# Kernel tuning notes

Measured on AMD Instinct MI355X. Metric: run time of the kernel, lower is better.

## Reference

```python
import jax, jax.numpy as jnp
import numpy as np

EMBED_DIM = 1024
NUM_HEAD = 16
HEAD_DIM = EMBED_DIM // NUM_HEAD


def _linear_params(key, in_dim, out_dim):
    kw, kb = jax.random.split(key)
    bound = 1.0 / np.sqrt(in_dim)
    W = jax.random.uniform(kw, (out_dim, in_dim), minval=-bound, maxval=bound, dtype=jnp.float32)
    b = jax.random.uniform(kb, (out_dim,), minval=-bound, maxval=bound, dtype=jnp.float32)
    return W, b


def setup_inputs() -> dict:
    key = jax.random.key(0)
    ks = jax.random.split(key, 7)
    N, S, E = 2, 2048, EMBED_DIM
    k = jax.random.normal(ks[0], (N, S, E), dtype=jnp.float32)
    q = jax.random.normal(ks[1], (N, S, E), dtype=jnp.float32)
    v = jax.random.normal(ks[2], (N, S, E), dtype=jnp.float32)
    Wk, bk = _linear_params(ks[3], E, E)
    Wq, bq = _linear_params(ks[4], E, E)
    Wv, bv = _linear_params(ks[5], E, E)
    Wo, bo = _linear_params(ks[6], E, E)
    return {"key": k, "query": q, "value": v,
            "Wk": Wk, "bk": bk, "Wq": Wq, "bq": bq,
            "Wv": Wv, "bv": bv, "Wo": Wo, "bo": bo}


def reference(key, query, value, Wk, bk, Wq, bq, Wv, bv, Wo, bo):
    N, S_in, E = key.shape
    S_out = query.shape[1]
    H, D = NUM_HEAD, HEAD_DIM
    # projections (torch Linear: x @ W.T + b), split heads -> [N, H, S, D]
    k = (key @ Wk.T + bk).reshape(N, S_in, H, D).transpose(0, 2, 1, 3)
    q = (query @ Wq.T + bq).reshape(N, S_out, H, D).transpose(0, 2, 1, 3)
    v = (value @ Wv.T + bv).reshape(N, S_in, H, D).transpose(0, 2, 1, 3)
    # unfused attention: full [N,H,S_out,S_in] score matrix, scale, softmax
    weight = jnp.einsum("nhqd,nhkd->nhqk", q, k) / jnp.sqrt(jnp.float32(D))
    weight = jax.nn.softmax(weight, axis=-1)
    attn = jnp.einsum("nhqk,nhkd->nhqd", weight, v)  # [N,H,S_out,D]
    attn = attn.transpose(0, 2, 1, 3).reshape(N, S_out, E)
    return attn @ Wo.T + bo
```

## Files before the change

### kernel.cpp

```cpp
#include <hip/hip_runtime.h>

constexpr int E  = 1024;
constexpr int NH = 16;
constexpr int HD = 64;
constexpr int S  = 2048;
constexpr int NB = 2;
constexpr int M  = NB * S;

typedef unsigned short u16;
typedef _Float16 f16;
typedef __attribute__((ext_vector_type(8))) _Float16 h8v;
typedef __attribute__((ext_vector_type(2))) __fp16 hp2v;
typedef __attribute__((ext_vector_type(4))) float f4v;

__device__ __forceinline__ f4v mfmaH(h8v a, h8v b, f4v c) {
    return __builtin_amdgcn_mfma_f32_16x16x32_f16(a, b, c, 0, 0, 0);
}
__device__ __forceinline__ u16 f16bits(float x) {
    union { f16 h; u16 u; } t; t.h = (f16)x; return t.u;
}
__device__ __forceinline__ unsigned pkrtz(float a, float b) {
    union { hp2v h; unsigned u; } t;
    t.h = __builtin_amdgcn_cvt_pkrtz(a, b);
    return t.u;
}
__device__ __forceinline__ float fexp2(float x) {
    float r;
    asm("v_exp_f32 %0, %1" : "=v"(r) : "v"(x));
    return r;
}
typedef const __attribute__((address_space(1))) void gvoid;
typedef __attribute__((address_space(3))) void lvoid;
__device__ __forceinline__ void load_lds16(const u16* g, u16* l) {
    __builtin_amdgcn_global_load_lds((gvoid*)g, (lvoid*)l, 16, 0, 0);
}

__global__ __launch_bounds__(256)
void cvt_f16(const float* __restrict__ q, const float* __restrict__ k,
             const float* __restrict__ v,
             const float* __restrict__ wq, const float* __restrict__ wk,
             const float* __restrict__ wv, const float* __restrict__ wo,
             u16* __restrict__ out)
{
    const size_t ME = (size_t)M * E, EE = (size_t)E * E;
    const int z = blockIdx.y;
    const float* src = (z == 0) ? q : (z == 1) ? k : (z == 2) ? v
                     : (z == 3) ? wq : (z == 4) ? wk : (z == 5) ? wv : wo;
    const size_t len = (z < 3) ? ME : EE;
    u16* dst = out + ((z < 3) ? (size_t)z * ME : 3 * ME + (size_t)(z - 3) * EE);
    for (size_t i = ((size_t)blockIdx.x * 256 + threadIdx.x) * 8; i < len;
         i += (size_t)gridDim.x * 256 * 8) {
        float4 a = *reinterpret_cast<const float4*>(src + i);
        float4 b = *reinterpret_cast<const float4*>(src + i + 4);
        h8v o;
        o[0] = (f16)a.x; o[1] = (f16)a.y; o[2] = (f16)a.z; o[3] = (f16)a.w;
        o[4] = (f16)b.x; o[5] = (f16)b.y; o[6] = (f16)b.z; o[7] = (f16)b.w;
        *reinterpret_cast<h8v*>(dst + i) = o;
    }
}

__device__ __forceinline__ void gemm16_core(const u16* __restrict__ A,
                                            const u16* __restrict__ W,
                                            int bm, int bn, u16* lds, f4v acc[4][4])
{
    const int tid  = threadIdx.x;
    const int lane = tid & 63;
    const int wid  = tid >> 6;
    const int g = lane >> 4, c = lane & 15;
    const int wr = wid >> 1, wc = wid & 1;
    const int lrow = lane >> 3;
    const int lslot = lane & 7;
    const int sslot = lslot ^ lrow;

    for (int k0 = 0; k0 < E; k0 += 64) {
        #pragma unroll
        for (int i = 0; i < 4; ++i) {
            int rbase = wid * 32 + i * 8;
            load_lds16(A + (size_t)(bm + rbase + lrow) * E + k0 + (sslot << 3),
                       &lds[rbase * 64]);
            load_lds16(W + (size_t)(bn + rbase + lrow) * E + k0 + (sslot << 3),
                       &lds[8192 + rbase * 64]);
        }
        __syncthreads();

        h8v a[4][2];
        #pragma unroll
        for (int mf = 0; mf < 4; ++mf) {
            int row = wr * 64 + mf * 16 + c;
            #pragma unroll
            for (int ks = 0; ks < 2; ++ks)
                a[mf][ks] = *reinterpret_cast<h8v*>(
                    &lds[row * 64 + ((((ks << 2) | g) ^ (c & 7)) << 3)]);
        }
        #pragma unroll
        for (int nf = 0; nf < 4; ++nf) {
            int row = wc * 64 + nf * 16 + c;
            #pragma unroll
            for (int ks = 0; ks < 2; ++ks) {
                h8v b = *reinterpret_cast<h8v*>(
                    &lds[8192 + row * 64 + ((((ks << 2) | g) ^ (c & 7)) << 3)]);
                #pragma unroll
                for (int mf = 0; mf < 4; ++mf)
                    acc[mf][nf] = mfmaH(a[mf][ks], b, acc[mf][nf]);
            }
        }
        __syncthreads();
    }
}

__global__ __launch_bounds__(256, 3)
void qkv_gemm(const u16* __restrict__ qf, const u16* __restrict__ kf,
              const u16* __restrict__ vf,
              const u16* __restrict__ wqf, const u16* __restrict__ wkf,
              const u16* __restrict__ wvf,
              const float* __restrict__ bq, const float* __restrict__ bk,
              const float* __restrict__ bv,
              u16* __restrict__ Qattn, u16* __restrict__ KV, float scaleQ)
{
    __shared__ __align__(16) u16 lds[16384];
    const int z = blockIdx.z;
    const u16* A = (z == 0) ? qf : (z == 1) ? kf : vf;
    const u16* W = (z == 0) ? wqf : (z == 1) ? wkf : wvf;
    const float* bias = (z == 0) ? bq : (z == 1) ? bk : bv;
    const float scl = (z == 0) ? scaleQ : 1.0f;
    const int bm = blockIdx.x * 128, bn = blockIdx.y * 128;

    f4v acc[4][4];
    #pragma unroll
    for (int a = 0; a < 4; ++a)
        #pragma unroll
        for (int b = 0; b < 4; ++b) acc[a][b] = (f4v){0.f, 0.f, 0.f, 0.f};

    gemm16_core(A, W, bm, bn, lds, acc);

    const int lane = threadIdx.x & 63;
    const int g = lane >> 4, c = lane & 15;
    const int wid = threadIdx.x >> 6;
    const int wr = wid >> 1, wc = wid & 1;
    float bcol[4];
    #pragma unroll
    for (int nf = 0; nf < 4; ++nf) bcol[nf] = bias[bn + wc * 64 + nf * 16 + c];

    #pragma unroll
    for (int mf = 0; mf < 4; ++mf)
        #pragma unroll
        for (int r = 0; r < 4; ++r) {
            int m  = bm + wr * 64 + mf * 16 + g * 4 + r;
            int nb = m >> 11, sp = m & (S - 1);
            #pragma unroll
            for (int nf = 0; nf < 4; ++nf) {
                int ncol = bn + wc * 64 + nf * 16 + c;
                int h = ncol >> 6, d = ncol & 63;
                int bh_ = nb * NH + h;
                u16 hb = f16bits((acc[mf][nf][r] + bcol[nf]) * scl);
                if (z == 0) {
                    Qattn[((size_t)bh_ * S + sp) * HD + d] = hb;
                } else if (z == 1) {
                    int t = sp >> 6, kk = (sp >> 4) & 3, cc = sp & 15;
                    int ds = d >> 5, gg = (d >> 3) & 3, j = d & 7;
                    KV[((size_t)bh_ * 32 + t) * 8192 +
                       ((size_t)((kk * 2 + ds) * 64 + gg * 16 + cc)) * 8 + j] = hb;
                } else {
                    int t = sp >> 6, rem = sp & 63;
                    int s2 = rem >> 5, bb = (rem >> 4) & 1, gg = (rem >> 2) & 3, a2 = rem & 3;
                    int j = 4 * bb + a2;
                    int df = d >> 4, cc = d & 15;
                    KV[((size_t)bh_ * 32 + t) * 8192 + 4096 +
                       ((size_t)((df * 2 + s2) * 64 + gg * 16 + cc)) * 8 + j] = hb;
                }
            }
        }
}

__global__ __launch_bounds__(256, 3)
void out_gemm(const u16* __restrict__ A, const u16* __restrict__ W,
              const float* __restrict__ bias, float* __restrict__ C)
{
    __shared__ __align__(16) u16 lds[16384];
    const int bm = blockIdx.x * 128, bn = blockIdx.y * 128;
    f4v acc[4][4];
    #pragma unroll
    for (int a = 0; a < 4; ++a)
        #pragma unroll
        for (int b = 0; b < 4; ++b) acc[a][b] = (f4v){0.f, 0.f, 0.f, 0.f};

    gemm16_core(A, W, bm, bn, lds, acc);

    const int lane = threadIdx.x & 63;
    const int g = lane >> 4, c = lane & 15;
    const int wid = threadIdx.x >> 6;
    const int wr = wid >> 1, wc = wid & 1;
    float bcol[4];
    #pragma unroll
    for (int nf = 0; nf < 4; ++nf) bcol[nf] = bias[bn + wc * 64 + nf * 16 + c];

    #pragma unroll
    for (int mf = 0; mf < 4; ++mf)
        #pragma unroll
        for (int r = 0; r < 4; ++r) {
            int m = bm + wr * 64 + mf * 16 + g * 4 + r;
            float* crow = &C[(size_t)m * E + bn + wc * 64];
            #pragma unroll
            for (int nf = 0; nf < 4; ++nf)
                crow[nf * 16 + c] = acc[mf][nf][r] + bcol[nf];
        }
}

__global__ __launch_bounds__(128, 2)
void attn_mfma(const u16* __restrict__ Qf, const u16* __restrict__ KV,
               u16* __restrict__ Out)
{
    __shared__ __align__(16) u16 lds[16384];
    const int tid  = threadIdx.x;
    const int lane = tid & 63;
    const int wid  = tid >> 6;
    const int g = lane >> 4, c = lane & 15;
    const int dlin = blockIdx.x;
    const int idx  = dlin >> 3;
    const int bh = (dlin & 7) * 4 + (idx >> 5);
    const int qc = idx & 31;
    const int n = bh >> 4, h = bh & 15;
    const int q0 = qc * 64 + wid * 32;
    const u16* kvb = KV + (size_t)bh * 32 * 8192;
    const f4v zero4 = {0.f, 0.f, 0.f, 0.f};

    h8v Qb[2][2];
    #pragma unroll
    for (int qf = 0; qf < 2; ++qf)
        #pragma unroll
        for (int ds = 0; ds < 2; ++ds)
            Qb[qf][ds] = *reinterpret_cast<const h8v*>(
                &Qf[((size_t)bh * S + q0 + qf * 16 + c) * HD + ds * 32 + g * 8]);

    h8v ones;
    #pragma unroll
    for (int i = 0; i < 8; ++i) ones[i] = (f16)1.0f;

    f4v oacc[2][4];
    #pragma unroll
    for (int qf = 0; qf < 2; ++qf)
        #pragma unroll
        for (int df = 0; df < 4; ++df) oacc[qf][df] = zero4;
    f4v lacc[2] = {zero4, zero4};

    f4v scA[2][4], scB[2][4];
    h8v vrA[4][2], vrB[4][2];

    #define STAGE(T, BUFOFF)                                                    \
    {                                                                           \
        const u16* src = kvb + (size_t)(T) * 8192 + wid * 4096 + lane * 8;      \
        u16* dst = &lds[(BUFOFF) + wid * 4096];                                 \
        _Pragma("unroll")                                                       \
        for (int i = 0; i < 8; ++i) load_lds16(src + i * 512, dst + i * 512);   \
    }

    STAGE(0, 0);
    STAGE(1, 8192);

    asm volatile("s_waitcnt vmcnt(8)" ::: "memory");
    __builtin_amdgcn_s_barrier();
    {
        const u16* Bt = &lds[0];
        #pragma unroll
        for (int qf = 0; qf < 2; ++qf)
            #pragma unroll
            for (int kf = 0; kf < 4; ++kf) scA[qf][kf] = zero4;
        __builtin_amdgcn_s_setprio(1);
        #pragma unroll
        for (int kf = 0; kf < 4; ++kf)
            #pragma unroll
            for (int ds = 0; ds < 2; ++ds) {
                h8v kh = *reinterpret_cast<const h8v*>(
                    &Bt[((size_t)((kf * 2 + ds) * 64 + lane)) * 8]);
                #pragma unroll
                for (int qf = 0; qf < 2; ++qf)
                    scA[qf][kf] = mfmaH(kh, Qb[qf][ds], scA[qf][kf]);
            }
        __builtin_amdgcn_s_setprio(0);
        #pragma unroll
        for (int df = 0; df < 4; ++df)
            #pragma unroll
            for (int s2 = 0; s2 < 2; ++s2)
                vrA[df][s2] = *reinterpret_cast<const h8v*>(
                    &Bt[4096 + ((size_t)((df * 2 + s2) * 64 + lane)) * 8]);
    }
    asm volatile("s_waitcnt lgkmcnt(0)" ::: "memory");
    __builtin_amdgcn_s_barrier();
    STAGE(2, 0);

    #define PHASE(T, BUFOFF, SCP, SCC, VRP, VRC, WAITN)                         \
    asm volatile("s_waitcnt vmcnt(" WAITN ")" ::: "memory");                    \
    __builtin_amdgcn_s_barrier();                                               \
    {                                                                           \
        const u16* Bt = &lds[BUFOFF];                                           \
        _Pragma("unroll")                                                       \
        for (int qf = 0; qf < 2; ++qf)                                          \
            _Pragma("unroll")                                                   \
            for (int kf = 0; kf < 4; ++kf) SCC[qf][kf] = zero4;                 \
        __builtin_amdgcn_s_setprio(1);                                          \
        _Pragma("unroll")                                                       \
        for (int kf = 0; kf < 4; ++kf)                                          \
            _Pragma("unroll")                                                   \
            for (int ds = 0; ds < 2; ++ds) {                                    \
                h8v kh = *reinterpret_cast<const h8v*>(                         \
                    &Bt[((size_t)((kf * 2 + ds) * 64 + lane)) * 8]);            \
                _Pragma("unroll")                                               \
                for (int qf = 0; qf < 2; ++qf)                                  \
                    SCC[qf][kf] = mfmaH(kh, Qb[qf][ds], SCC[qf][kf]);           \
            }                                                                   \
        __builtin_amdgcn_s_setprio(0);                                          \
        h8v pah[2][2];                                                          \
        _Pragma("unroll")                                                       \
        for (int qf = 0; qf < 2; ++qf)                                          \
            _Pragma("unroll")                                                   \
            for (int s2 = 0; s2 < 2; ++s2) {                                    \
                union { h8v v; unsigned u[4]; } th;                             \
                _Pragma("unroll")                                               \
                for (int kfh = 0; kfh < 2; ++kfh) {                             \
                    int kf = 2 * s2 + kfh;                                      \
                    float p0 = fexp2(SCP[qf][kf][0]);                           \
                    float p1 = fexp2(SCP[qf][kf][1]);                           \
                    float p2 = fexp2(SCP[qf][kf][2]);                           \
                    float p3 = fexp2(SCP[qf][kf][3]);                           \
                    th.u[2 * kfh + 0] = pkrtz(p0, p1);                          \
                    th.u[2 * kfh + 1] = pkrtz(p2, p3);                          \
                }                                                               \
                pah[qf][s2] = th.v;                                             \
            }                                                                   \
        __builtin_amdgcn_s_setprio(1);                                          \
        _Pragma("unroll")                                                       \
        for (int qf = 0; qf < 2; ++qf) {                                        \
            lacc[qf] = mfmaH(pah[qf][0], ones, lacc[qf]);                       \
            lacc[qf] = mfmaH(pah[qf][1], ones, lacc[qf]);                       \
        }                                                                       \
        _Pragma("unroll")                                                       \
        for (int df = 0; df < 4; ++df)                                          \
            _Pragma("unroll")                                                   \
            for (int s2 = 0; s2 < 2; ++s2)                                      \
                _Pragma("unroll")                                               \
                for (int qf = 0; qf < 2; ++qf)                                  \
                    oacc[qf][df] = mfmaH(pah[qf][s2], VRP[df][s2],              \
                                         oacc[qf][df]);                         \
        __builtin_amdgcn_s_setprio(0);                                          \
        _Pragma("unroll")                                                       \
        for (int df = 0; df < 4; ++df)                                          \
            _Pragma("unroll")                                                   \
            for (int s2 = 0; s2 < 2; ++s2)                                      \
                VRC[df][s2] = *reinterpret_cast<const h8v*>(                    \
                    &Bt[4096 + ((size_t)((df * 2 + s2) * 64 + lane)) * 8]);     \
    }                                                                           \
    asm volatile("s_waitcnt lgkmcnt(0)" ::: "memory");                          \
    __builtin_amdgcn_s_barrier();                                               \
    if ((T) + 2 < 32) STAGE((T) + 2, BUFOFF)

    for (int t = 1; t < 31; t += 2) {
        PHASE(t,     8192, scA, scB, vrA, vrB, "8");
        PHASE(t + 1, 0,    scB, scA, vrB, vrA, "8");
    }
    PHASE(31, 8192, scA, scB, vrA, vrB, "0");
    #undef PHASE
    #undef STAGE

    {
        h8v pah[2][2];
        #pragma unroll
        for (int qf = 0; qf < 2; ++qf)
            #pragma unroll
            for (int s2 = 0; s2 < 2; ++s2) {
                union { h8v v; unsigned u[4]; } th;
                #pragma unroll
                for (int kfh = 0; kfh < 2; ++kfh) {
                    int kf = 2 * s2 + kfh;
                    float p0 = fexp2(scB[qf][kf][0]);
                    float p1 = fexp2(scB[qf][kf][1]);
                    float p2 = fexp2(scB[qf][kf][2]);
                    float p3 = fexp2(scB[qf][kf][3]);
                    th.u[2 * kfh + 0] = pkrtz(p0, p1);
                    th.u[2 * kfh + 1] = pkrtz(p2, p3);
                }
                pah[qf][s2] = th.v;
            }
        #pragma unroll
        for (int qf = 0; qf < 2; ++qf) {
            lacc[qf] = mfmaH(pah[qf][0], ones, lacc[qf]);
            lacc[qf] = mfmaH(pah[qf][1], ones, lacc[qf]);
        }
        #pragma unroll
        for (int df = 0; df < 4; ++df)
            #pragma unroll
            for (int s2 = 0; s2 < 2; ++s2)
                #pragma unroll
                for (int qf = 0; qf < 2; ++qf)
                    oacc[qf][df] = mfmaH(pah[qf][s2], vrB[df][s2], oacc[qf][df]);
    }

    #pragma unroll
    for (int qf = 0; qf < 2; ++qf)
        #pragma unroll
        for (int r = 0; r < 4; ++r) {
            float linv = 1.0f / lacc[qf][r];
            int q = q0 + qf * 16 + g * 4 + r;
            size_t ob = ((size_t)n * S + q) * E + h * HD;
            #pragma unroll
            for (int df = 0; df < 4; ++df)
                Out[ob + df * 16 + c] = f16bits(oacc[qf][df][r] * linv);
        }
}

extern "C" void kernel_launch(void* const* d_in, const int* in_sizes, int n_in,
                              void* d_out, int out_size, void* d_ws, size_t ws_size,
                              hipStream_t stream)
{
    const float* key   = (const float*)d_in[0];
    const float* query = (const float*)d_in[1];
    const float* value = (const float*)d_in[2];
    const float* Wk    = (const float*)d_in[3];
    const float* bk    = (const float*)d_in[4];
    const float* Wq    = (const float*)d_in[5];
    const float* bq    = (const float*)d_in[6];
    const float* Wv    = (const float*)d_in[7];
    const float* bv    = (const float*)d_in[8];
    const float* Wo    = (const float*)d_in[9];
    const float* bo    = (const float*)d_in[10];

    const size_t ME = (size_t)M * E, EE = (size_t)E * E;
    u16* ws16  = (u16*)d_ws;
    u16* qf16  = ws16;
    u16* kf16  = ws16 + ME;
    u16* vf16  = ws16 + 2 * ME;
    u16* wqf   = ws16 + 3 * ME;
    u16* wkf   = wqf + EE;
    u16* wvf   = wkf + EE;
    u16* wof   = wvf + EE;
    u16* Qattn = wof + EE;
    u16* KV    = Qattn + ME;
    u16* AoutH = ws16;

    const float SCALE_Q = 0.125f * 1.44269504088896340736f;

    cvt_f16<<<dim3(2048, 7), 256, 0, stream>>>(query, key, value, Wq, Wk, Wv, Wo, ws16);
    qkv_gemm<<<dim3(M / 128, E / 128, 3), 256, 0, stream>>>(
        qf16, kf16, vf16, wqf, wkf, wvf, bq, bk, bv, Qattn, KV, SCALE_Q);
    attn_mfma<<<dim3((S / 64) * NB * NH), 128, 0, stream>>>(Qattn, KV, AoutH);
    out_gemm<<<dim3(M / 128, E / 128), 256, 0, stream>>>(AoutH, wof, bo, (float*)d_out);
}
```

Baseline: 115.4 us.

## Load V tiles directly from global into registers, staging only K through LDS

The attention kernel now stages only the K half of each KV tile into LDS and fetches V fragments straight from global memory into registers one tile ahead. This halves the LDS buffer and removes the LDS round trip and lgkmcnt waits for V, and the vmcnt thresholds are adjusted to match. In exchange, V comes in through per-lane global loads whose latency has to be hidden within a single phase. It also raises vector-memory pressure and makes correctness depend on the new wait-count bookkeeping.

```diff
diff --git a/kernel.cpp b/kernel.cpp
--- a/kernel.cpp
+++ b/kernel.cpp
@@ -210,7 +210,7 @@
 void attn_mfma(const u16* __restrict__ Qf, const u16* __restrict__ KV,
                u16* __restrict__ Out)
 {
-    __shared__ __align__(16) u16 lds[16384];
+    __shared__ __align__(16) u16 lds[8192];
     const int tid  = threadIdx.x;
     const int lane = tid & 63;
     const int wid  = tid >> 6;
@@ -246,18 +246,29 @@
     f4v scA[2][4], scB[2][4];
     h8v vrA[4][2], vrB[4][2];
 
-    #define STAGE(T, BUFOFF)                                                    \
+    #define STAGE_K(T, BUFOFF)                                                  \
     {                                                                           \
-        const u16* src = kvb + (size_t)(T) * 8192 + wid * 4096 + lane * 8;      \
-        u16* dst = &lds[(BUFOFF) + wid * 4096];                                 \
-        _Pragma("unroll")                                                       \
-        for (int i = 0; i < 8; ++i) load_lds16(src + i * 512, dst + i * 512);   \
-    }
-
-    STAGE(0, 0);
-    STAGE(1, 8192);
-
-    asm volatile("s_waitcnt vmcnt(8)" ::: "memory");
+        const u16* src = kvb + (size_t)(T) * 8192 + wid * 2048 + lane * 8;      \
+        u16* dst = &lds[(BUFOFF) + wid * 2048];                                 \
+        _Pragma("unroll")                                                       \
+        for (int i = 0; i < 4; ++i) load_lds16(src + i * 512, dst + i * 512);   \
+    }
+    #define VLOAD(T, VR)                                                        \
+    {                                                                           \
+        _Pragma("unroll")                                                       \
+        for (int df = 0; df < 4; ++df)                                          \
+            _Pragma("unroll")                                                   \
+            for (int s2 = 0; s2 < 2; ++s2)                                      \
+                VR[df][s2] = *reinterpret_cast<const h8v*>(                     \
+                    &kvb[(size_t)(T) * 8192 + 4096 +                            \
+                         ((size_t)((df * 2 + s2) * 64 + lane)) * 8]);           \
+    }
+
+    VLOAD(0, vrA);
+    STAGE_K(0, 0);
+    STAGE_K(1, 4096);
+
+    asm volatile("s_waitcnt vmcnt(4)" ::: "memory");
     __builtin_amdgcn_s_barrier();
     {
         const u16* Bt = &lds[0];
@@ -277,18 +288,12 @@
                     scA[qf][kf] = mfmaH(kh, Qb[qf][ds], scA[qf][kf]);
             }
         __builtin_amdgcn_s_setprio(0);
-        #pragma unroll
-        for (int df = 0; df < 4; ++df)
-            #pragma unroll
-            for (int s2 = 0; s2 < 2; ++s2)
-                vrA[df][s2] = *reinterpret_cast<const h8v*>(
-                    &Bt[4096 + ((size_t)((df * 2 + s2) * 64 + lane)) * 8]);
-    }
-    asm volatile("s_waitcnt lgkmcnt(0)" ::: "memory");
+        VLOAD(1, vrB);
+    }
     __builtin_amdgcn_s_barrier();
-    STAGE(2, 0);
-
-    #define PHASE(T, BUFOFF, SCP, SCC, VRP, VRC, WAITN)                         \
+    STAGE_K(2, 0);
+
+    #define PHASE(T, BUFOFF, SCP, SCC, VOLD, WAITN)                             \
     asm volatile("s_waitcnt vmcnt(" WAITN ")" ::: "memory");                    \
     __builtin_amdgcn_s_barrier();                                               \
     {                                                                           \
@@ -339,27 +344,22 @@
             for (int s2 = 0; s2 < 2; ++s2)                                      \
                 _Pragma("unroll")                                               \
                 for (int qf = 0; qf < 2; ++qf)                                  \
-                    oacc[qf][df] = mfmaH(pah[qf][s2], VRP[df][s2],              \
+                    oacc[qf][df] = mfmaH(pah[qf][s2], VOLD[df][s2],             \
                                          oacc[qf][df]);                         \
         __builtin_amdgcn_s_setprio(0);                                          \
-        _Pragma("unroll")                                                       \
-        for (int df = 0; df < 4; ++df)                                          \
-            _Pragma("unroll")                                                   \
-            for (int s2 = 0; s2 < 2; ++s2)                                      \
-                VRC[df][s2] = *reinterpret_cast<const h8v*>(                    \
-                    &Bt[4096 + ((size_t)((df * 2 + s2) * 64 + lane)) * 8]);     \
+        if ((T) + 1 < 32) VLOAD((T) + 1, VOLD);                                 \
     }                                                                           \
-    asm volatile("s_waitcnt lgkmcnt(0)" ::: "memory");                          \
     __builtin_amdgcn_s_barrier();                                               \
-    if ((T) + 2 < 32) STAGE((T) + 2, BUFOFF)
+    if ((T) + 2 < 32) STAGE_K((T) + 2, BUFOFF)
 
     for (int t = 1; t < 31; t += 2) {
-        PHASE(t,     8192, scA, scB, vrA, vrB, "8");
-        PHASE(t + 1, 0,    scB, scA, vrB, vrA, "8");
-    }
-    PHASE(31, 8192, scA, scB, vrA, vrB, "0");
+        PHASE(t,     4096, scA, scB, vrA, "12");
+        PHASE(t + 1, 0,    scB, scA, vrB, "12");
+    }
+    PHASE(31, 4096, scA, scB, vrA, "8");
     #undef PHASE
-    #undef STAGE
+    #undef STAGE_K
+    #undef VLOAD
 
     {
         h8v pah[2][2];
```

Result: no change. 116.0 us (+0.5%).
